# Optimization experiments

Hardware: AMD Instinct MI355X
Metric: run time of the kernel (lower is better)

Reference implementation:

```python
import jax, jax.numpy as jnp
import numpy as np

N_NODES = 50000
N_EDGES = 800000
D_IN = 96
HID = 128


def _glorot(key, shape):
    fan_in, fan_out = shape[0], shape[1]
    lim = np.sqrt(6.0 / (fan_in + fan_out)).astype(np.float32)
    return jax.random.uniform(key, shape, jnp.float32, -lim, lim)


def setup_inputs() -> dict:
    key = jax.random.key(0)
    ks = jax.random.split(key, 12)
    x = jax.random.normal(ks[0], (N_NODES, D_IN), jnp.float32)
    edge_index = jax.random.randint(ks[1], (2, N_EDGES), 0, N_NODES)
    return {
        "x": x,
        "edge_index": edge_index,
        "W_in": _glorot(ks[2], (D_IN, HID)),
        "b_in": jnp.zeros((HID,), jnp.float32),
        "W1": _glorot(ks[3], (HID, HID)),
        "b1": jnp.zeros((HID,), jnp.float32),
        "W2": _glorot(ks[4], (HID, HID)),
        "b2": jnp.zeros((HID,), jnp.float32),
        "Wm1": _glorot(ks[5], (2 * HID, HID)),
        "bm1": jnp.zeros((HID,), jnp.float32),
        "Wm2": _glorot(ks[6], (HID, 1)),
        "bm2": jnp.zeros((1,), jnp.float32),
    }


def _gcn_conv(h, W, b, src, dst, n_nodes):
    # PyG GCNConv with add_self_loops=True, normalize=True:
    # out = D^{-1/2} (A + I) D^{-1/2} (h W) + b, aggregating x_j (source) into dst.
    loop = jnp.arange(n_nodes)
    row = jnp.concatenate([src, loop])  # source / j
    col = jnp.concatenate([dst, loop])  # target / i
    deg = jax.ops.segment_sum(jnp.ones(row.shape, h.dtype), col, num_segments=n_nodes)
    dinv = jnp.where(deg > 0, jax.lax.rsqrt(deg), 0.0)
    norm = dinv[row] * dinv[col]  # [E+N]
    xw = h @ W  # [N, H]
    msg = xw[row] * norm[:, None]  # gather + scale, [E+N, H]
    out = jax.ops.segment_sum(msg, col, num_segments=n_nodes)  # scatter-add
    return out + b


def reference(x, edge_index, W_in, b_in, W1, b1, W2, b2, Wm1, bm1, Wm2, bm2):
    src, dst = edge_index[0], edge_index[1]
    n = x.shape[0]
    h = jax.nn.relu(x @ W_in + b_in)  # dropout is identity at inference
    h = jax.nn.relu(_gcn_conv(h, W1, b1, src, dst, n))
    h = jax.nn.relu(_gcn_conv(h, W2, b2, src, dst, n))
    ef = jnp.concatenate([h[src], h[dst]], axis=1)  # [E, 2H]
    hid = jax.nn.relu(ef @ Wm1 + bm1)
    logits = (hid @ Wm2 + bm2)[:, 0]  # [E]
    return logits
```

## Files before the change

### kernel.cpp

```cpp
#include <hip/hip_runtime.h>

#define N_NODES 50000
#define N_EDGES 800000
#define D_IN 96
#define HID 128
#define NB 391
#define BCAP 3072
#define AECAP 768

typedef __attribute__((ext_vector_type(8))) _Float16 halfx8;
typedef __attribute__((ext_vector_type(4))) _Float16 half4v;
typedef __attribute__((ext_vector_type(2))) _Float16 half2v;
typedef __attribute__((ext_vector_type(16))) float f32x16;

__device__ inline float dot2acc(half2v a, half2v b, float c) {
#if __has_builtin(__builtin_amdgcn_fdot2)
    return __builtin_amdgcn_fdot2(a, b, c, false);
#else
    return c + (float)a[0] * (float)b[0] + (float)a[1] * (float)b[1];
#endif
}

__device__ inline halfx8 relu8(halfx8 s) {
#if __has_builtin(__builtin_elementwise_max)
    return __builtin_elementwise_max(s, (halfx8)0);
#else
    halfx8 r;
#pragma unroll
    for (int i = 0; i < 8; i++) r[i] = s[i] > (_Float16)0 ? s[i] : (_Float16)0;
    return r;
#endif
}

__global__ __launch_bounds__(256) void hist_pack_kernel(const int* __restrict__ dst,
                                                        int* __restrict__ bhist,
                                                        const float* __restrict__ W_in,
                                                        const float* __restrict__ W1,
                                                        const float* __restrict__ W2,
                                                        const float* __restrict__ Wm1,
                                                        const float* __restrict__ Wm2,
                                                        _Float16* __restrict__ packed) {
    __shared__ int lh[NB];
    int t = threadIdx.x;
    if (blockIdx.x < 196) {
        for (int i = t; i < NB; i += 256) lh[i] = 0;
        __syncthreads();
        int base = blockIdx.x * 4096;
#pragma unroll
        for (int i = 0; i < 16; i++) {
            int e = base + i * 256 + t;
            if (e < N_EDGES) atomicAdd(&lh[dst[e] >> 7], 1);
        }
        __syncthreads();
        for (int i = t; i < NB; i += 256) atomicAdd(&bhist[i], lh[i]);
        return;
    }
    int g = (blockIdx.x - 196) * 256 + t;
    if (g >= 77952) return;
    if (g >= 77824) { packed[g] = (_Float16)Wm2[g - 77824]; return; }
    const float* Wsrc;
    int K, u;
    if (g < 12288)      { Wsrc = W_in;            K = 96;  u = g; }
    else if (g < 28672) { Wsrc = W1;              K = 128; u = g - 12288; }
    else if (g < 45056) { Wsrc = W2;              K = 128; u = g - 28672; }
    else if (g < 61440) { Wsrc = Wm1;             K = 128; u = g - 45056; }
    else                { Wsrc = Wm1 + 128 * 128; K = 128; u = g - 61440; }
    int steps = K >> 4;
    int cb = u / (steps * 512);
    int rem = u - cb * steps * 512;
    int s = rem >> 9;
    int lane = (rem >> 3) & 63;
    int j = rem & 7;
    int k = s * 16 + ((lane >> 5) << 3) + j;
    int n = (cb << 5) + (lane & 31);
    packed[g] = (_Float16)Wsrc[k * 128 + n];
}

__global__ __launch_bounds__(512) void scan_buckets_kernel(const int* __restrict__ bhist,
                                                           int* __restrict__ boff,
                                                           int* __restrict__ bcursor) {
    __shared__ int s[512];
    int t = threadIdx.x;
    int v = (t < NB) ? bhist[t] : 0;
    s[t] = v;
    __syncthreads();
    for (int off = 1; off < 512; off <<= 1) {
        int u = (t >= off) ? s[t - off] : 0;
        __syncthreads();
        s[t] += u;
        __syncthreads();
    }
    if (t < NB) {
        int ex = s[t] - v;
        boff[t] = ex;
        bcursor[t] = ex;
    }
    if (t == NB - 1) boff[NB] = s[t];
}

__global__ __launch_bounds__(512) void bin_kernel(const int* __restrict__ src,
                                                  const int* __restrict__ dst,
                                                  int* __restrict__ bcursor,
                                                  unsigned long long* __restrict__ binned) {
    __shared__ int lh[NB];
    __shared__ int gbs[NB];
    int t = threadIdx.x;
    for (int i = t; i < NB; i += 512) lh[i] = 0;
    __syncthreads();
    int base = blockIdx.x * 8192;
    unsigned long long pk[16];
    int bb[16], rk[16];
#pragma unroll
    for (int i = 0; i < 16; i++) {
        int e = base + i * 512 + t;
        bb[i] = -1;
        if (e < N_EDGES) {
            int s = src[e], d = dst[e];
            int b = d >> 7;
            bb[i] = b;
            pk[i] = ((unsigned long long)s << 27) |
                    ((unsigned long long)(d & 127) << 20) | (unsigned long long)e;
            rk[i] = atomicAdd(&lh[b], 1);
        }
    }
    __syncthreads();
    for (int i = t; i < NB; i += 512) gbs[i] = atomicAdd(&bcursor[i], lh[i]);
    __syncthreads();
#pragma unroll
    for (int i = 0; i < 16; i++) {
        if (bb[i] >= 0) binned[gbs[bb[i]] + rk[i]] = pk[i];
    }
}

__global__ __launch_bounds__(256) void bucket_sort_kernel(const unsigned long long* __restrict__ binned,
                                                          const int* __restrict__ boff,
                                                          int* __restrict__ ce_src,
                                                          int* __restrict__ ce_eid,
                                                          int* __restrict__ ce_dst,
                                                          int* __restrict__ csr_ptr,
                                                          float* __restrict__ dinv) {
    __shared__ int2 sorted[BCAP];
    __shared__ int cntA[128], sc[128];
    int b = blockIdx.x;
    int t = threadIdx.x;
    int base = boff[b];
    int k = boff[b + 1] - base;
    if (k > BCAP) k = BCAP;
    if (t < 128) cntA[t] = 0;
    __syncthreads();
    unsigned long long pk[12];
    int rk[12];
#pragma unroll
    for (int m = 0; m < 12; m++) {
        int i = t + m * 256;
        rk[m] = -1;
        if (i < k) {
            unsigned long long p = binned[base + i];
            pk[m] = p;
            int d = (int)((p >> 20) & 127);
            rk[m] = atomicAdd(&cntA[d], 1);
        }
    }
    __syncthreads();
    if (t < 128) sc[t] = cntA[t];
    __syncthreads();
    for (int off = 1; off < 128; off <<= 1) {
        int u = 0;
        if (t < 128 && t >= off) u = sc[t - off];
        __syncthreads();
        if (t < 128) sc[t] += u;
        __syncthreads();
    }
#pragma unroll
    for (int m = 0; m < 12; m++) {
        if (rk[m] >= 0) {
            unsigned long long p = pk[m];
            int d = (int)((p >> 20) & 127);
            int pos = sc[d] - cntA[d] + rk[m];
            int srcn = (int)(p >> 27);
            int eid = (int)(p & 0xFFFFF);
            sorted[pos] = make_int2(srcn | (d << 16), eid);
        }
    }
    __syncthreads();
    for (int i = t; i < k; i += 256) {
        int2 se = sorted[i];
        ce_src[base + i] = se.x & 0xFFFF;
        ce_eid[base + i] = se.y;
        ce_dst[base + i] = (b << 7) + (se.x >> 16);
    }
    if (t < 128) {
        int node = (b << 7) + t;
        if (node < N_NODES) {
            csr_ptr[node] = base + sc[t] - cntA[t];
            dinv[node] = 1.0f / sqrtf((float)(cntA[t] + 1));
        }
    }
    if (b == NB - 1 && t == 0) csr_ptr[N_NODES] = boff[NB];
}

__global__ __launch_bounds__(256) void fused_in_kernel(const float* __restrict__ x,
                                                       const _Float16* __restrict__ WpIn,
                                                       const _Float16* __restrict__ Wp1,
                                                       const float* __restrict__ b_in,
                                                       const float* __restrict__ dinv,
                                                       _Float16* __restrict__ y1, int M) {
    __shared__ _Float16 As[32 * 104];
    __shared__ _Float16 Hs[32 * 136];
    int tid = threadIdx.x;
    int M0 = blockIdx.x * 32;
    for (int i = tid; i < 32 * 24; i += 256) {
        int r = i / 24, c = i - r * 24;
        float4 v = make_float4(0.f, 0.f, 0.f, 0.f);
        int row = M0 + r;
        if (row < M) v = *(const float4*)&x[(size_t)row * 96 + c * 4];
        half2v a = {(_Float16)v.x, (_Float16)v.y};
        half2v b = {(_Float16)v.z, (_Float16)v.w};
        *(half2v*)&As[r * 104 + c * 4] = a;
        *(half2v*)&As[r * 104 + c * 4 + 2] = b;
    }
    __syncthreads();

    int wave = tid >> 6, lane = tid & 63;
    int col = wave * 32 + (lane & 31);
    {
        const halfx8* bp = (const halfx8*)WpIn + (size_t)wave * 6 * 64 + lane;
        const _Float16* arow = &As[(lane & 31) * 104 + ((lane >> 5) << 3)];
        f32x16 acc = {};
#pragma unroll
        for (int s = 0; s < 6; s++) {
            halfx8 a = *(const halfx8*)&arow[s * 16];
            acc = __builtin_amdgcn_mfma_f32_32x32x16_f16(a, bp[s * 64], acc, 0, 0, 0);
        }
        float bA = b_in[col];
#pragma unroll
        for (int r = 0; r < 16; r++) {
            int rl = (r & 3) + 8 * (r >> 2) + 4 * (lane >> 5);
            Hs[rl * 136 + col] = (_Float16)fmaxf(acc[r] + bA, 0.f);
        }
    }
    __syncthreads();
    {
        const halfx8* bp = (const halfx8*)Wp1 + (size_t)wave * 8 * 64 + lane;
        const _Float16* arow = &Hs[(lane & 31) * 136 + ((lane >> 5) << 3)];
        f32x16 acc = {};
#pragma unroll
        for (int s = 0; s < 8; s++) {
            halfx8 a = *(const halfx8*)&arow[s * 16];
            acc = __builtin_amdgcn_mfma_f32_32x32x16_f16(a, bp[s * 64], acc, 0, 0, 0);
        }
#pragma unroll
        for (int r = 0; r < 16; r++) {
            int rl = (r & 3) + 8 * (r >> 2) + 4 * (lane >> 5);
            int grow = M0 + rl;
            if (grow < M) {
                y1[((size_t)wave * N_NODES + grow) * 32 + (lane & 31)] =
                    (_Float16)(acc[r] * dinv[grow]);
            }
        }
    }
}

__global__ __launch_bounds__(256) void gemm_f16_kernel(const _Float16* __restrict__ A,
                                                       const _Float16* __restrict__ Wp,
                                                       const float* __restrict__ bias,
                                                       const float* __restrict__ rowscale,
                                                       _Float16* __restrict__ out,
                                                       int M, int steps, int dorelu) {
    const int K = 128;
    __shared__ _Float16 As[32 * 136];
    int tid = threadIdx.x;
    int M0 = blockIdx.x * 32;
    int stride = K + 8;
    for (int i = tid; i < 32 * 16; i += 256) {
        int r = i >> 4, c = i & 15;
        uint4 v = make_uint4(0, 0, 0, 0);
        int row = M0 + r;
        if (row < M)
            v = *(const uint4*)&A[((size_t)(c >> 2) * N_NODES + row) * 32 + (c & 3) * 8];
        *(uint4*)&As[r * stride + c * 8] = v;
    }
    __syncthreads();

    int wave = tid >> 6, lane = tid & 63;
    const halfx8* bp = (const halfx8*)Wp + (size_t)wave * steps * 64 + lane;
    const _Float16* arow = &As[(lane & 31) * stride + ((lane >> 5) << 3)];
    f32x16 acc = {};
    for (int s = 0; s < steps; s++) {
        halfx8 a = *(const halfx8*)&arow[s * 16];
        acc = __builtin_amdgcn_mfma_f32_32x32x16_f16(a, bp[s * 64], acc, 0, 0, 0);
    }
    int col = wave * 32 + (lane & 31);
    float bA = bias ? bias[col] : 0.f;
#pragma unroll
    for (int r = 0; r < 16; r++) {
        int rl = (r & 3) + 8 * (r >> 2) + 4 * (lane >> 5);
        int grow = M0 + rl;
        if (grow < M) {
            float sc = rowscale ? rowscale[grow] : 1.f;
            float v0 = (acc[r] + bA) * sc;
            if (dorelu) v0 = fmaxf(v0, 0.f);
            out[((size_t)wave * N_NODES + grow) * 32 + (lane & 31)] = (_Float16)v0;
        }
    }
}

__global__ __launch_bounds__(256) void gemm_uv_kernel(const _Float16* __restrict__ A,
                                                      const _Float16* __restrict__ WpU,
                                                      const _Float16* __restrict__ WpV,
                                                      const float* __restrict__ bm1,
                                                      _Float16* __restrict__ U,
                                                      _Float16* __restrict__ V,
                                                      int M) {
    const int K = 128, steps = 8;
    __shared__ _Float16 As[32 * 136];
    int tid = threadIdx.x;
    int M0 = blockIdx.x * 32;
    int stride = K + 8;
    for (int i = tid; i < 32 * 16; i += 256) {
        int r = i >> 4, c = i & 15;
        uint4 v = make_uint4(0, 0, 0, 0);
        int row = M0 + r;
        if (row < M)
            v = *(const uint4*)&A[((size_t)(c >> 2) * N_NODES + row) * 32 + (c & 3) * 8];
        *(uint4*)&As[r * stride + c * 8] = v;
    }
    __syncthreads();

    int wave = tid >> 6, lane = tid & 63;
    const halfx8* bu = (const halfx8*)WpU + (size_t)wave * steps * 64 + lane;
    const halfx8* bv = (const halfx8*)WpV + (size_t)wave * steps * 64 + lane;
    const _Float16* arow = &As[(lane & 31) * stride + ((lane >> 5) << 3)];
    f32x16 au = {}, av = {};
#pragma unroll
    for (int s = 0; s < steps; s++) {
        halfx8 a = *(const halfx8*)&arow[s * 16];
        au = __builtin_amdgcn_mfma_f32_32x32x16_f16(a, bu[s * 64], au, 0, 0, 0);
        av = __builtin_amdgcn_mfma_f32_32x32x16_f16(a, bv[s * 64], av, 0, 0, 0);
    }
    int col = wave * 32 + (lane & 31);
    float bA = bm1[col];
#pragma unroll
    for (int r = 0; r < 16; r++) {
        int rl = (r & 3) + 8 * (r >> 2) + 4 * (lane >> 5);
        int grow = M0 + rl;
        if (grow < M) {
            U[(size_t)grow * 128 + col] = (_Float16)(au[r] + bA);
            V[(size_t)grow * 128 + col] = (_Float16)av[r];
        }
    }
}

__global__ __launch_bounds__(256, 6) void aggregate_kernel(const _Float16* __restrict__ y,
                                                           const float* __restrict__ dinv,
                                                           const int* __restrict__ ptr,
                                                           const int* __restrict__ ce_src,
                                                           const float* __restrict__ bias,
                                                           _Float16* __restrict__ out) {
    __shared__ int sidx[AECAP];
    __shared__ int sptr[17];
    int b = blockIdx.x;
    int sl = (b & 7) >> 1;
    int o = ((b >> 3) << 1) + (b & 1);
    if (o >= 3125) return;
    int node0 = o * 16;
    int tid = threadIdx.x;
    if (tid < 17) sptr[tid] = ptr[node0 + tid];
    __syncthreads();
    int base = sptr[0];
    int tot = sptr[16] - base;
    bool fit = (tot <= AECAP);
    if (fit) {
        for (int i = tid; i < tot; i += 256) sidx[i] = ce_src[base + i];
    }
    __syncthreads();

    int g = tid >> 4;
    int l = tid & 15;
    int node = node0 + g;
    float di = dinv[node];
    const _Float16* ys = y + (size_t)sl * N_NODES * 32 + l * 2;
    half2v self = *(const half2v*)&ys[(size_t)node * 32];
    float a0 = (float)self[0], a1 = (float)self[1];
    float b0 = 0.f, b1 = 0.f;
    int s0 = sptr[g], s1 = sptr[g + 1];

    if (fit) {
        int j = s0 - base, e = s1 - base;
        while (j < e) {
            half2v v[16];
#pragma unroll
            for (int k = 0; k < 16; k++) {
                int idx = j + k;
                int n = sidx[idx < e ? idx : e - 1];
                v[k] = *(const half2v*)&ys[(size_t)n * 32];
            }
            __builtin_amdgcn_sched_barrier(0);
#pragma unroll
            for (int k = 0; k < 16; k += 2) {
                float m0 = (j + k < e) ? 1.f : 0.f;
                float m1 = (j + k + 1 < e) ? 1.f : 0.f;
                a0 += m0 * (float)v[k][0];     a1 += m0 * (float)v[k][1];
                b0 += m1 * (float)v[k + 1][0]; b1 += m1 * (float)v[k + 1][1];
            }
            j += 16;
        }
    } else {
        for (int j = s0; j < s1; j++) {
            int n = ce_src[j];
            half2v v = *(const half2v*)&ys[(size_t)n * 32];
            a0 += (float)v[0]; a1 += (float)v[1];
        }
    }
    float2 bv = *(const float2*)&bias[sl * 32 + l * 2];
    half2v ov;
    ov[0] = (_Float16)fmaxf(di * (a0 + b0) + bv.x, 0.f);
    ov[1] = (_Float16)fmaxf(di * (a1 + b1) + bv.y, 0.f);
    *(half2v*)&out[((size_t)sl * N_NODES + node) * 32 + l * 2] = ov;
}

__global__ __launch_bounds__(256) void edge_mlp_kernel(const _Float16* __restrict__ Ub,
                                                       const _Float16* __restrict__ Vb,
                                                       const int* __restrict__ ce_src,
                                                       const int* __restrict__ ce_eid,
                                                       const int* __restrict__ ce_dst,
                                                       const _Float16* __restrict__ Wm2h,
                                                       const float* __restrict__ bm2,
                                                       float* __restrict__ out) {
    __shared__ int ssrc[128], sdst[128], seid[128];
    int tid = threadIdx.x;
    int e0 = blockIdx.x * 128;
    if (tid < 128) {
        ssrc[tid] = ce_src[e0 + tid];
        seid[tid] = ce_eid[e0 + tid];
    } else {
        sdst[tid - 128] = ce_dst[e0 + tid - 128];
    }
    __syncthreads();
    int g = tid >> 4;
    int l = tid & 15;
    halfx8 wv = *(const halfx8*)&Wm2h[l * 8];
    half2v w0 = {wv[0], wv[1]}, w1 = {wv[2], wv[3]}, w2 = {wv[4], wv[5]}, w3 = {wv[6], wv[7]};
    halfx8 uu[8], vv[8];
#pragma unroll
    for (int k = 0; k < 8; k++) {
        int e = g + 16 * k;
        uu[k] = *(const halfx8*)&Ub[(size_t)ssrc[e] * 128 + l * 8];
        vv[k] = *(const halfx8*)&Vb[(size_t)sdst[e] * 128 + l * 8];
    }
    __builtin_amdgcn_sched_barrier(0);
    float p[8];
#pragma unroll
    for (int k = 0; k < 8; k++) {
        halfx8 s = relu8(uu[k] + vv[k]);
        half2v s0 = {s[0], s[1]}, s1 = {s[2], s[3]}, s2 = {s[4], s[5]}, s3 = {s[6], s[7]};
        float acc = dot2acc(s0, w0, 0.f);
        acc = dot2acc(s1, w1, acc);
        acc = dot2acc(s2, w2, acc);
        p[k] = dot2acc(s3, w3, acc);
    }
#pragma unroll
    for (int d = 1; d < 16; d <<= 1) {
#pragma unroll
        for (int k = 0; k < 8; k++) p[k] += __shfl_xor(p[k], d);
    }
    if (l == 0) {
        float bb = bm2[0];
#pragma unroll
        for (int k = 0; k < 8; k++) out[seid[g + 16 * k]] = p[k] + bb;
    }
}

extern "C" void kernel_launch(void* const* d_in, const int* in_sizes, int n_in,
                              void* d_out, int out_size, void* d_ws, size_t ws_size,
                              hipStream_t stream) {
    const float* x    = (const float*)d_in[0];
    const int* eidx   = (const int*)d_in[1];
    const float* W_in = (const float*)d_in[2];
    const float* b_in = (const float*)d_in[3];
    const float* W1   = (const float*)d_in[4];
    const float* b1   = (const float*)d_in[5];
    const float* W2   = (const float*)d_in[6];
    const float* b2   = (const float*)d_in[7];
    const float* Wm1  = (const float*)d_in[8];
    const float* bm1  = (const float*)d_in[9];
    const float* Wm2  = (const float*)d_in[10];
    const float* bm2  = (const float*)d_in[11];
    float* out = (float*)d_out;
    const int* src = eidx;
    const int* dst = eidx + N_EDGES;

    char* w = (char*)d_ws;
    size_t off = 0;
    auto alloc = [&](size_t bytes) -> char* {
        char* p = w + off;
        off = (off + bytes + 255) & ~(size_t)255;
        return p;
    };
    int* bhist    = (int*)alloc((size_t)NB * 4);
    int* boff     = (int*)alloc((size_t)(NB + 1) * 4);
    int* bcursor  = (int*)alloc((size_t)NB * 4);
    int* csr_ptr  = (int*)alloc((size_t)(N_NODES + 1) * 4);
    float* dinv   = (float*)alloc((size_t)N_NODES * 4);
    unsigned long long* binned = (unsigned long long*)alloc((size_t)N_EDGES * 8);
    int* ce_src   = (int*)alloc((size_t)N_EDGES * 4);
    int* ce_eid   = (int*)alloc((size_t)N_EDGES * 4);
    int* ce_dst   = (int*)alloc((size_t)N_EDGES * 4);
    _Float16* Wp  = (_Float16*)alloc((size_t)77952 * 2);
    _Float16* y1  = (_Float16*)alloc((size_t)N_NODES * HID * 2);
    _Float16* y2  = (_Float16*)alloc((size_t)N_NODES * HID * 2);
    _Float16* hbuf = (_Float16*)alloc((size_t)N_NODES * HID * 2);
    _Float16* Ub  = (_Float16*)alloc((size_t)N_NODES * HID * 2);
    _Float16* Vb  = (_Float16*)alloc((size_t)N_NODES * HID * 2);

    const _Float16* WpIn  = Wp;
    const _Float16* Wp1   = Wp + 12288;
    const _Float16* Wp2   = Wp + 28672;
    const _Float16* WpM1a = Wp + 45056;
    const _Float16* WpM1b = Wp + 61440;
    const _Float16* Wm2h  = Wp + 77824;

    hipMemsetAsync(bhist, 0, (size_t)NB * 4, stream);
    hist_pack_kernel<<<196 + 305, 256, 0, stream>>>(dst, bhist, W_in, W1, W2, Wm1, Wm2, Wp);
    scan_buckets_kernel<<<1, 512, 0, stream>>>(bhist, boff, bcursor);
    bin_kernel<<<98, 512, 0, stream>>>(src, dst, bcursor, binned);
    bucket_sort_kernel<<<NB, 256, 0, stream>>>(binned, boff, ce_src, ce_eid, ce_dst,
                                               csr_ptr, dinv);

    int gblocks = (N_NODES + 31) / 32;
    int ablocks = 1563 * 8;
    fused_in_kernel<<<gblocks, 256, 0, stream>>>(x, WpIn, Wp1, b_in, dinv, y1, N_NODES);
    aggregate_kernel<<<ablocks, 256, 0, stream>>>(y1, dinv, csr_ptr, ce_src, b1, hbuf);
    gemm_f16_kernel<<<gblocks, 256, 0, stream>>>(hbuf, Wp2, nullptr, dinv, y2,
                                                 N_NODES, 8, 0);
    aggregate_kernel<<<ablocks, 256, 0, stream>>>(y2, dinv, csr_ptr, ce_src, b2, hbuf);
    gemm_uv_kernel<<<gblocks, 256, 0, stream>>>(hbuf, WpM1a, WpM1b, bm1, Ub, Vb, N_NODES);
    edge_mlp_kernel<<<N_EDGES / 128, 256, 0, stream>>>(Ub, Vb, ce_src, ce_eid, ce_dst,
                                                       Wm2h, bm2, out);
}
```

Before: 269.8 us.

## Remap aggregate kernel to 16-byte vector gathers with 64 nodes per block

```diff
diff --git a/kernel.cpp b/kernel.cpp
--- a/kernel.cpp
+++ b/kernel.cpp
@@ -6,7 +6,7 @@
 #define HID 128
 #define NB 391
 #define BCAP 3072
-#define AECAP 768
+#define AECAP 1408
 
 typedef __attribute__((ext_vector_type(8))) _Float16 halfx8;
 typedef __attribute__((ext_vector_type(4))) _Float16 half4v;
@@ -358,65 +358,107 @@
                                                            const float* __restrict__ bias,
                                                            _Float16* __restrict__ out) {
     __shared__ int sidx[AECAP];
-    __shared__ int sptr[17];
+    __shared__ int sptr[65];
     int b = blockIdx.x;
     int sl = (b & 7) >> 1;
     int o = ((b >> 3) << 1) + (b & 1);
-    if (o >= 3125) return;
-    int node0 = o * 16;
+    int node0 = o * 64;
     int tid = threadIdx.x;
-    if (tid < 17) sptr[tid] = ptr[node0 + tid];
+    if (tid < 65) {
+        int nn = node0 + tid;
+        sptr[tid] = ptr[nn < N_NODES ? nn : N_NODES];
+    }
     __syncthreads();
     int base = sptr[0];
-    int tot = sptr[16] - base;
+    int tot = sptr[64] - base;
     bool fit = (tot <= AECAP);
     if (fit) {
-        for (int i = tid; i < tot; i += 256) sidx[i] = ce_src[base + i];
-    }
-    __syncthreads();
-
-    int g = tid >> 4;
-    int l = tid & 15;
-    int node = node0 + g;
+        for (int i = tid; i < tot; i += 256) sidx[i] = ce_src[base + i] << 6;
+    }
+    __syncthreads();
+
+    int g = tid >> 2;
+    int l = tid & 3;
+    int nodeIdx = node0 + g;
+    int node = nodeIdx < N_NODES ? nodeIdx : N_NODES - 1;
     float di = dinv[node];
-    const _Float16* ys = y + (size_t)sl * N_NODES * 32 + l * 2;
-    half2v self = *(const half2v*)&ys[(size_t)node * 32];
-    float a0 = (float)self[0], a1 = (float)self[1];
-    float b0 = 0.f, b1 = 0.f;
+    const char* ysl = (const char*)y + (size_t)sl * (N_NODES * 64) + (size_t)l * 16;
+    halfx8 self = *(const halfx8*)(ysl + (size_t)node * 64);
+    float a0 = (float)self[0], a1 = (float)self[1], a2 = (float)self[2], a3 = (float)self[3];
+    float a4 = (float)self[4], a5 = (float)self[5], a6 = (float)self[6], a7 = (float)self[7];
     int s0 = sptr[g], s1 = sptr[g + 1];
 
     if (fit) {
         int j = s0 - base, e = s1 - base;
-        while (j < e) {
-            half2v v[16];
-#pragma unroll
-            for (int k = 0; k < 16; k++) {
-                int idx = j + k;
-                int n = sidx[idx < e ? idx : e - 1];
-                v[k] = *(const half2v*)&ys[(size_t)n * 32];
-            }
+        for (; j + 7 < e; j += 8) {
+            halfx8 v0 = *(const halfx8*)(ysl + sidx[j]);
+            halfx8 v1 = *(const halfx8*)(ysl + sidx[j + 1]);
+            halfx8 v2 = *(const halfx8*)(ysl + sidx[j + 2]);
+            halfx8 v3 = *(const halfx8*)(ysl + sidx[j + 3]);
+            halfx8 v4 = *(const halfx8*)(ysl + sidx[j + 4]);
+            halfx8 v5 = *(const halfx8*)(ysl + sidx[j + 5]);
+            halfx8 v6 = *(const halfx8*)(ysl + sidx[j + 6]);
+            halfx8 v7 = *(const halfx8*)(ysl + sidx[j + 7]);
             __builtin_amdgcn_sched_barrier(0);
-#pragma unroll
-            for (int k = 0; k < 16; k += 2) {
-                float m0 = (j + k < e) ? 1.f : 0.f;
-                float m1 = (j + k + 1 < e) ? 1.f : 0.f;
-                a0 += m0 * (float)v[k][0];     a1 += m0 * (float)v[k][1];
-                b0 += m1 * (float)v[k + 1][0]; b1 += m1 * (float)v[k + 1][1];
-            }
-            j += 16;
+            a0 += (float)v0[0] + (float)v1[0] + (float)v2[0] + (float)v3[0]
+                + (float)v4[0] + (float)v5[0] + (float)v6[0] + (float)v7[0];
+            a1 += (float)v0[1] + (float)v1[1] + (float)v2[1] + (float)v3[1]
+                + (float)v4[1] + (float)v5[1] + (float)v6[1] + (float)v7[1];
+            a2 += (float)v0[2] + (float)v1[2] + (float)v2[2] + (float)v3[2]
+                + (float)v4[2] + (float)v5[2] + (float)v6[2] + (float)v7[2];
+            a3 += (float)v0[3] + (float)v1[3] + (float)v2[3] + (float)v3[3]
+                + (float)v4[3] + (float)v5[3] + (float)v6[3] + (float)v7[3];
+            a4 += (float)v0[4] + (float)v1[4] + (float)v2[4] + (float)v3[4]
+                + (float)v4[4] + (float)v5[4] + (float)v6[4] + (float)v7[4];
+            a5 += (float)v0[5] + (float)v1[5] + (float)v2[5] + (float)v3[5]
+                + (float)v4[5] + (float)v5[5] + (float)v6[5] + (float)v7[5];
+            a6 += (float)v0[6] + (float)v1[6] + (float)v2[6] + (float)v3[6]
+                + (float)v4[6] + (float)v5[6] + (float)v6[6] + (float)v7[6];
+            a7 += (float)v0[7] + (float)v1[7] + (float)v2[7] + (float)v3[7]
+                + (float)v4[7] + (float)v5[7] + (float)v6[7] + (float)v7[7];
+        }
+        for (; j + 3 < e; j += 4) {
+            halfx8 v0 = *(const halfx8*)(ysl + sidx[j]);
+            halfx8 v1 = *(const halfx8*)(ysl + sidx[j + 1]);
+            halfx8 v2 = *(const halfx8*)(ysl + sidx[j + 2]);
+            halfx8 v3 = *(const halfx8*)(ysl + sidx[j + 3]);
+            __builtin_amdgcn_sched_barrier(0);
+            a0 += (float)v0[0] + (float)v1[0] + (float)v2[0] + (float)v3[0];
+            a1 += (float)v0[1] + (float)v1[1] + (float)v2[1] + (float)v3[1];
+            a2 += (float)v0[2] + (float)v1[2] + (float)v2[2] + (float)v3[2];
+            a3 += (float)v0[3] + (float)v1[3] + (float)v2[3] + (float)v3[3];
+            a4 += (float)v0[4] + (float)v1[4] + (float)v2[4] + (float)v3[4];
+            a5 += (float)v0[5] + (float)v1[5] + (float)v2[5] + (float)v3[5];
+            a6 += (float)v0[6] + (float)v1[6] + (float)v2[6] + (float)v3[6];
+            a7 += (float)v0[7] + (float)v1[7] + (float)v2[7] + (float)v3[7];
+        }
+        for (; j < e; j++) {
+            halfx8 v = *(const halfx8*)(ysl + sidx[j]);
+            a0 += (float)v[0]; a1 += (float)v[1]; a2 += (float)v[2]; a3 += (float)v[3];
+            a4 += (float)v[4]; a5 += (float)v[5]; a6 += (float)v[6]; a7 += (float)v[7];
         }
     } else {
         for (int j = s0; j < s1; j++) {
-            int n = ce_src[j];
-            half2v v = *(const half2v*)&ys[(size_t)n * 32];
-            a0 += (float)v[0]; a1 += (float)v[1];
-        }
-    }
-    float2 bv = *(const float2*)&bias[sl * 32 + l * 2];
-    half2v ov;
-    ov[0] = (_Float16)fmaxf(di * (a0 + b0) + bv.x, 0.f);
-    ov[1] = (_Float16)fmaxf(di * (a1 + b1) + bv.y, 0.f);
-    *(half2v*)&out[((size_t)sl * N_NODES + node) * 32 + l * 2] = ov;
+            halfx8 v = *(const halfx8*)(ysl + ((size_t)ce_src[j] << 6));
+            a0 += (float)v[0]; a1 += (float)v[1]; a2 += (float)v[2]; a3 += (float)v[3];
+            a4 += (float)v[4]; a5 += (float)v[5]; a6 += (float)v[6]; a7 += (float)v[7];
+        }
+    }
+    if (nodeIdx < N_NODES) {
+        const float* bp = &bias[sl * 32 + l * 8];
+        float4 bv0 = *(const float4*)bp;
+        float4 bv1 = *(const float4*)(bp + 4);
+        halfx8 ov;
+        ov[0] = (_Float16)fmaxf(di * a0 + bv0.x, 0.f);
+        ov[1] = (_Float16)fmaxf(di * a1 + bv0.y, 0.f);
+        ov[2] = (_Float16)fmaxf(di * a2 + bv0.z, 0.f);
+        ov[3] = (_Float16)fmaxf(di * a3 + bv0.w, 0.f);
+        ov[4] = (_Float16)fmaxf(di * a4 + bv1.x, 0.f);
+        ov[5] = (_Float16)fmaxf(di * a5 + bv1.y, 0.f);
+        ov[6] = (_Float16)fmaxf(di * a6 + bv1.z, 0.f);
+        ov[7] = (_Float16)fmaxf(di * a7 + bv1.w, 0.f);
+        *(halfx8*)&out[((size_t)sl * N_NODES + nodeIdx) * 32 + l * 8] = ov;
+    }
 }
 
 __global__ __launch_bounds__(256) void edge_mlp_kernel(const _Float16* __restrict__ Ub,
@@ -528,7 +570,7 @@
                                                csr_ptr, dinv);
 
     int gblocks = (N_NODES + 31) / 32;
-    int ablocks = 1563 * 8;
+    int ablocks = 782 * 4;
     fused_in_kernel<<<gblocks, 256, 0, stream>>>(x, WpIn, Wp1, b_in, dinv, y1, N_NODES);
     aggregate_kernel<<<ablocks, 256, 0, stream>>>(y1, dinv, csr_ptr, ce_src, b1, hbuf);
     gemm_f16_kernel<<<gblocks, 256, 0, stream>>>(hbuf, Wp2, nullptr, dinv, y2,
```

Measured after the change: 238.3 us. 11.7% less time.
